# Kernel tuning notes

Measured on AMD Instinct MI355X. Metric: run time of the kernel, lower is better.

Reference implementation:

```python
import jax, jax.numpy as jnp
import numpy as np

D = 2048      # d_model
H = 32        # n_heads
DS = 64       # d_state = d_model // n_heads
K = 4         # conv kernel size (hardcoded in module)
EPS = 1e-6


def setup_inputs() -> dict:
    key = jax.random.key(0)
    ks = jax.random.split(key, 8)
    B, L = 2, 4096
    s = lambda k, shp, sc: jax.random.normal(k, shp, dtype=jnp.float32) * sc
    return {
        "x": s(ks[0], (B, L, D), 1.0),
        "state": jnp.zeros((B, H, DS), jnp.float32),
        "norm_w": jnp.ones((D,), jnp.float32),
        "conv_w": s(ks[1], (D, K), 0.5),          # depthwise conv weight [d_model, K]
        "conv_b": s(ks[2], (D,), 0.1),
        "pp_w": s(ks[3], (D, 3 * H * DS), 0.02),  # param_proj (stored [in, out])
        "pp_b": jnp.zeros((3 * H * DS,), jnp.float32),
        "gp_w": s(ks[4], (D, D), 0.02),           # gate_proj
        "gp_b": jnp.zeros((D,), jnp.float32),
        "op_w": s(ks[5], (D, D), 0.02),           # out_proj
        "op_b": jnp.zeros((D,), jnp.float32),
    }


def reference(x, state, norm_w, conv_w, conv_b, pp_w, pp_b, gp_w, gp_b, op_w, op_b):
    B, L, Dm = x.shape
    # RMSNorm
    rms = jnp.sqrt(jnp.mean(x * x, axis=-1, keepdims=True) + EPS)
    xn = norm_w * x / rms
    # causal depthwise conv1d + SiLU (pad left K-1, valid cross-correlation)
    xp = jnp.pad(xn, ((0, 0), (K - 1, 0), (0, 0)))
    xc = conv_b + sum(xp[:, k:k + L, :] * conv_w[:, k] for k in range(K))
    xc = jax.nn.silu(xc)
    gate = jax.nn.sigmoid(xc @ gp_w + gp_b)                  # [B, L, D]
    p = (xn @ pp_w + pp_b).reshape(B, L, H, 3, DS)
    delta = jax.nn.sigmoid(p[..., 0, :])                     # [B, L, H, DS]
    Bm, Cm = p[..., 1, :], p[..., 2, :]
    # sequential recurrence h_t = delta_t * h_{t-1} + B_t, time-major scan
    dt = jnp.moveaxis(delta, 1, 0)                           # [L, B, H, DS]
    Bt = jnp.moveaxis(Bm, 1, 0)
    def step(h, db):
        d, b = db
        h = d * h + b
        return h, h
    h_last, hs = jax.lax.scan(step, state, (dt, Bt))         # hs: [L, B, H, DS]
    ssm = (jnp.moveaxis(Cm, 1, 0) * hs).reshape(L, B, Dm)
    ssm = jnp.moveaxis(ssm, 0, 1)                            # [B, L, D]
    mixed = gate * ssm + (1.0 - gate) * xn
    y = mixed @ op_w + op_b + x
    return y, h_last
```

## Files before the change

### kernel.cpp

```cpp
#include <hip/hip_runtime.h>
#include <math.h>

#define BB   2
#define LL   4096
#define DD   2048
#define HH   32
#define DSS  64
#define MM   (BB * LL)
#define N3   (3 * HH * DSS)
#define NCH  64
#define CLN  64
#define EPSF 1e-6f

typedef unsigned short bf16;
typedef __attribute__((ext_vector_type(8))) short bf16x8;
typedef __attribute__((ext_vector_type(4))) float f32x4;

__device__ __forceinline__ float bf2f(bf16 u) {
    union { unsigned int i; float f; } v;
    v.i = ((unsigned int)u) << 16;
    return v.f;
}
__device__ __forceinline__ bf16 f2bf(float f) {
    union { float f; unsigned int u; } v;
    v.f = f;
    unsigned int r = (v.u >> 16) & 1u;
    return (bf16)((v.u + 0x7fffu + r) >> 16);
}
__device__ __forceinline__ float sigmoidf_(float v) {
    return 1.0f / (1.0f + __expf(-v));
}
__device__ __forceinline__ void gload16(const void* g, void* l) {
    __builtin_amdgcn_global_load_lds(
        (const __attribute__((address_space(1))) void*)g,
        (__attribute__((address_space(3))) void*)l, 16, 0, 0);
}

__global__ __launch_bounds__(256) void rms_kernel(const float* __restrict__ x,
                                                  const float* __restrict__ w,
                                                  bf16* __restrict__ xn) {
    int row = blockIdx.x;
    const float4* x4 = (const float4*)(x + (size_t)row * DD);
    ushort4* o4 = (ushort4*)(xn + (size_t)row * DD);
    const float4* w4 = (const float4*)w;
    int t = threadIdx.x;
    float4 v0 = x4[t], v1 = x4[t + 256];
    float ss = v0.x * v0.x + v0.y * v0.y + v0.z * v0.z + v0.w * v0.w +
               v1.x * v1.x + v1.y * v1.y + v1.z * v1.z + v1.w * v1.w;
#pragma unroll
    for (int off = 32; off >= 1; off >>= 1) ss += __shfl_down(ss, off, 64);
    __shared__ float red[4];
    if ((t & 63) == 0) red[t >> 6] = ss;
    __syncthreads();
    float tot = red[0] + red[1] + red[2] + red[3];
    float inv = 1.0f / sqrtf(tot * (1.0f / DD) + EPSF);
    float4 wa = w4[t], wb = w4[t + 256];
    ushort4 r0, r1;
    r0.x = f2bf(v0.x * inv * wa.x); r0.y = f2bf(v0.y * inv * wa.y);
    r0.z = f2bf(v0.z * inv * wa.z); r0.w = f2bf(v0.w * inv * wa.w);
    r1.x = f2bf(v1.x * inv * wb.x); r1.y = f2bf(v1.y * inv * wb.y);
    r1.z = f2bf(v1.z * inv * wb.z); r1.w = f2bf(v1.w * inv * wb.w);
    o4[t] = r0; o4[t + 256] = r1;
}

__global__ __launch_bounds__(256) void conv_silu_kernel(const bf16* __restrict__ xn,
                                                        const float* __restrict__ cw,
                                                        const float* __restrict__ cb,
                                                        bf16* __restrict__ xc) {
    int l = blockIdx.x;
    int b = blockIdx.y;
    size_t base = ((size_t)b * LL + l) * DD;
#pragma unroll
    for (int i = 0; i < 8; ++i) {
        int d = (i << 8) + threadIdx.x;
        float4 w = ((const float4*)cw)[d];
        float acc = cb[d];
        if (l >= 3) {
            acc += bf2f(xn[base - 3 * (size_t)DD + d]) * w.x +
                   bf2f(xn[base - 2 * (size_t)DD + d]) * w.y +
                   bf2f(xn[base - 1 * (size_t)DD + d]) * w.z +
                   bf2f(xn[base + d]) * w.w;
        } else {
            const float wv[4] = {w.x, w.y, w.z, w.w};
#pragma unroll
            for (int k = 0; k < 4; ++k) {
                int ls = l - 3 + k;
                if (ls >= 0) acc += bf2f(xn[((size_t)b * LL + ls) * DD + d]) * wv[k];
            }
        }
        xc[base + d] = f2bf(acc * sigmoidf_(acc));
    }
}

__global__ __launch_bounds__(256) void transpose_bf(const float* __restrict__ W,
                                                    bf16* __restrict__ WT,
                                                    int Kdim, int Ndim) {
    __shared__ float t[32][33];
    int n0 = blockIdx.x << 5, k0 = blockIdx.y << 5;
    int tx = threadIdx.x & 31;
    int ty = threadIdx.x >> 5;
#pragma unroll
    for (int i = 0; i < 32; i += 8)
        t[ty + i][tx] = W[(size_t)(k0 + ty + i) * Ndim + n0 + tx];
    __syncthreads();
#pragma unroll
    for (int i = 0; i < 32; i += 8)
        WT[(size_t)(n0 + ty + i) * Kdim + k0 + tx] = f2bf(t[tx][ty + i]);
}

template <int EPI, typename OutT>
__global__ __launch_bounds__(256) void gemm_mfma(const bf16* __restrict__ A,
                                                 const bf16* __restrict__ Bt,
                                                 const float* __restrict__ bias,
                                                 const float* __restrict__ add,
                                                 OutT* __restrict__ out,
                                                 int Ndim, int Kdim) {
    __shared__ __align__(16) bf16 As[128 * 64];
    __shared__ __align__(16) bf16 Bs[128 * 64];
    const int tid  = threadIdx.x;
    const int wave = tid >> 6;
    const int lane = tid & 63;
    const int m0 = blockIdx.y << 7;
    const int n0 = blockIdx.x << 7;

    const int sr = lane >> 3;
    const int gcol = ((lane & 7) ^ sr) << 3;
    const bf16* gA[4];
    const bf16* gB[4];
    bf16* lA[4];
    bf16* lB[4];
#pragma unroll
    for (int p = 0; p < 4; ++p) {
        int c = wave * 4 + p;
        gA[p] = A  + (size_t)(m0 + c * 8 + sr) * Kdim + gcol;
        gB[p] = Bt + (size_t)(n0 + c * 8 + sr) * Kdim + gcol;
        lA[p] = As + c * 512 + lane * 8;
        lB[p] = Bs + c * 512 + lane * 8;
    }

    const int wm = (wave >> 1) << 6;
    const int wn = (wave & 1) << 6;
    const int fr = lane & 15;
    const int kg = lane >> 4;
    const int f7 = fr & 7;

    f32x4 acc[4][4] = {};
    for (int k0 = 0; k0 < Kdim; k0 += 64) {
        __syncthreads();
#pragma unroll
        for (int p = 0; p < 4; ++p) {
            gload16(gA[p] + k0, lA[p]);
            gload16(gB[p] + k0, lB[p]);
        }
        __syncthreads();
#pragma unroll
        for (int ks = 0; ks < 2; ++ks) {
            bf16x8 af[4], bf_[4];
#pragma unroll
            for (int i = 0; i < 4; ++i) {
                int gq = (((ks << 2) | kg) ^ f7) << 3;
                af[i]  = *(const bf16x8*)&As[(wm + i * 16 + fr) * 64 + gq];
                bf_[i] = *(const bf16x8*)&Bs[(wn + i * 16 + fr) * 64 + gq];
            }
#pragma unroll
            for (int i = 0; i < 4; ++i)
#pragma unroll
                for (int j = 0; j < 4; ++j)
                    acc[i][j] = __builtin_amdgcn_mfma_f32_16x16x32_bf16(
                        af[i], bf_[j], acc[i][j], 0, 0, 0);
        }
    }

    const int baseRow = m0 + wm + kg * 4;
    const int baseCol = n0 + wn + fr;
#pragma unroll
    for (int i = 0; i < 4; ++i) {
#pragma unroll
        for (int r = 0; r < 4; ++r) {
            int m = baseRow + i * 16 + r;
            size_t rowoff = (size_t)m * Ndim + baseCol;
#pragma unroll
            for (int j = 0; j < 4; ++j) {
                float v = acc[i][j][r] + bias[baseCol + j * 16];
                if (EPI == 1) v = sigmoidf_(v);
                if (EPI == 2) v += add[rowoff + j * 16];
                if constexpr (sizeof(OutT) == 4)
                    ((float*)out)[rowoff + j * 16] = v;
                else
                    ((bf16*)out)[rowoff + j * 16] = f2bf(v);
            }
        }
    }
}


__global__ __launch_bounds__(256) void scan_phase1(const bf16* __restrict__ p,
                                                   float* __restrict__ cA,
                                                   float* __restrict__ cB) {
    int c = blockIdx.x, b = blockIdx.z, s = threadIdx.x & 63;
    int h = blockIdx.y * 4 + (threadIdx.x >> 6);
    size_t base = ((size_t)(b * LL + c * CLN)) * N3 + h * (3 * DSS) + s;
    float a = 1.0f, bb = 0.0f;
    for (int i = 0; i < CLN; ++i) {
        float d = sigmoidf_(bf2f(p[base]));
        float Bv = bf2f(p[base + DSS]);
        a *= d;
        bb = d * bb + Bv;
        base += N3;
    }
    int idx = ((b * HH + h) * NCH + c) * DSS + s;
    cA[idx] = a;
    cB[idx] = bb;
}

__global__ __launch_bounds__(64) void scan_phase2(const float* __restrict__ state,
                                                  const float* __restrict__ cA,
                                                  const float* __restrict__ cB,
                                                  float* __restrict__ cH,
                                                  float* __restrict__ hlast) {
    int h = blockIdx.x, b = blockIdx.y, s = threadIdx.x;
    float hp = state[(b * HH + h) * DSS + s];
    int base = ((b * HH + h) * NCH) * DSS + s;
    for (int c = 0; c < NCH; ++c) {
        cH[base + c * DSS] = hp;
        hp = cA[base + c * DSS] * hp + cB[base + c * DSS];
    }
    hlast[(b * HH + h) * DSS + s] = hp;
}

__global__ __launch_bounds__(256) void scan_phase3(const bf16* __restrict__ p,
                                                   const float* __restrict__ cH,
                                                   const bf16* __restrict__ gate,
                                                   const bf16* __restrict__ xn,
                                                   bf16* __restrict__ mixed) {
    int c = blockIdx.x, b = blockIdx.z, s = threadIdx.x & 63;
    int h = blockIdx.y * 4 + (threadIdx.x >> 6);
    float hp = cH[((b * HH + h) * NCH + c) * DSS + s];
    size_t prow = ((size_t)(b * LL + c * CLN)) * N3 + h * (3 * DSS) + s;
    size_t grow = ((size_t)(b * LL + c * CLN)) * DD + h * DSS + s;
    for (int i = 0; i < CLN; ++i) {
        float d = sigmoidf_(bf2f(p[prow]));
        float Bv = bf2f(p[prow + DSS]);
        float Cv = bf2f(p[prow + 2 * DSS]);
        hp = d * hp + Bv;
        float ssm = Cv * hp;
        float g = bf2f(gate[grow]);
        float xv = bf2f(xn[grow]);
        mixed[grow] = f2bf(g * ssm + (1.0f - g) * xv);
        prow += N3;
        grow += DD;
    }
}

extern "C" void kernel_launch(void* const* d_in, const int* in_sizes, int n_in,
                              void* d_out, int out_size, void* d_ws, size_t ws_size,
                              hipStream_t stream) {
    const float* x      = (const float*)d_in[0];
    const float* state  = (const float*)d_in[1];
    const float* norm_w = (const float*)d_in[2];
    const float* conv_w = (const float*)d_in[3];
    const float* conv_b = (const float*)d_in[4];
    const float* pp_w   = (const float*)d_in[5];
    const float* pp_b   = (const float*)d_in[6];
    const float* gp_w   = (const float*)d_in[7];
    const float* gp_b   = (const float*)d_in[8];
    const float* op_w   = (const float*)d_in[9];
    const float* op_b   = (const float*)d_in[10];

    float* y     = (float*)d_out;
    float* hlast = y + (size_t)MM * DD;

    const size_t BHND = (size_t)BB * HH * NCH * DSS;
    char* ws = (char*)d_ws;
    bf16* xn    = (bf16*)ws;
    bf16* xcbuf = xn + (size_t)MM * DD;
    bf16* p     = xcbuf + (size_t)MM * DD;
    float* cA   = (float*)(p + (size_t)MM * N3);
    float* cB   = cA + BHND;
    float* cH   = cB + BHND;
    bf16* gp_wT = (bf16*)(cH + BHND);
    bf16* op_wT = gp_wT + (size_t)DD * DD;
    bf16* pp_wT = xcbuf;
    bf16* gate  = (bf16*)y;
    bf16* mixed = xcbuf;

    rms_kernel<<<MM, 256, 0, stream>>>(x, norm_w, xn);
    conv_silu_kernel<<<dim3(LL, BB), 256, 0, stream>>>(xn, conv_w, conv_b, xcbuf);
    transpose_bf<<<dim3(DD / 32, DD / 32), 256, 0, stream>>>(gp_w, gp_wT, DD, DD);
    gemm_mfma<1, bf16><<<dim3(DD / 128, MM / 128), 256, 0, stream>>>(
        xcbuf, gp_wT, gp_b, nullptr, gate, DD, DD);
    transpose_bf<<<dim3(N3 / 32, DD / 32), 256, 0, stream>>>(pp_w, pp_wT, DD, N3);
    gemm_mfma<0, bf16><<<dim3(N3 / 128, MM / 128), 256, 0, stream>>>(
        xn, pp_wT, pp_b, nullptr, p, N3, DD);
    scan_phase1<<<dim3(NCH, HH / 4, BB), 256, 0, stream>>>(p, cA, cB);
    scan_phase2<<<dim3(HH, BB), 64, 0, stream>>>(state, cA, cB, cH, hlast);
    scan_phase3<<<dim3(NCH, HH / 4, BB), 256, 0, stream>>>(p, cH, gate, xn, mixed);
    transpose_bf<<<dim3(DD / 32, DD / 32), 256, 0, stream>>>(op_w, op_wT, DD, DD);
    gemm_mfma<2, float><<<dim3(DD / 128, MM / 128), 256, 0, stream>>>(
        mixed, op_wT, op_b, x, y, DD, DD);
}
```

Baseline: 701.2 us.

## Fuse gate and param projection GEMMs, merge weight transposes, stream conv along L

The gate-projection and param-projection GEMMs now run as a single launch, with blocks dispatched by column index, and the three weight transposes are combined into one kernel. The depthwise conv now walks 32 timesteps per thread with a register sliding window and 4-wide vector loads, so each input row is not reloaded four times. The pp_wT scratch buffer moves into the unused half of the output buffer so that it no longer aliases xc. The aims are fewer launches, better GPU fill, and less redundant memory traffic in the conv; the costs are more complex buffer aliasing and lower parallelism in the conv grid.

```diff
diff --git a/kernel.cpp b/kernel.cpp
--- a/kernel.cpp
+++ b/kernel.cpp
@@ -11,6 +11,8 @@
 #define NCH  64
 #define CLN  64
 #define EPSF 1e-6f
+#define GP_NB (DD / 128)
+#define PP_NB (N3 / 128)
 
 typedef unsigned short bf16;
 typedef __attribute__((ext_vector_type(8))) short bf16x8;
@@ -63,40 +65,67 @@
     o4[t] = r0; o4[t + 256] = r1;
 }
 
+#define CONV_LC 32
 __global__ __launch_bounds__(256) void conv_silu_kernel(const bf16* __restrict__ xn,
                                                         const float* __restrict__ cw,
                                                         const float* __restrict__ cb,
                                                         bf16* __restrict__ xc) {
-    int l = blockIdx.x;
-    int b = blockIdx.y;
-    size_t base = ((size_t)b * LL + l) * DD;
-#pragma unroll
-    for (int i = 0; i < 8; ++i) {
-        int d = (i << 8) + threadIdx.x;
-        float4 w = ((const float4*)cw)[d];
-        float acc = cb[d];
-        if (l >= 3) {
-            acc += bf2f(xn[base - 3 * (size_t)DD + d]) * w.x +
-                   bf2f(xn[base - 2 * (size_t)DD + d]) * w.y +
-                   bf2f(xn[base - 1 * (size_t)DD + d]) * w.z +
-                   bf2f(xn[base + d]) * w.w;
+    int b = blockIdx.z;
+    int l0 = blockIdx.x * CONV_LC;
+    int d0 = blockIdx.y * 1024 + threadIdx.x * 4;
+    float4 w[4];
+    float bias[4];
+#pragma unroll
+    for (int j = 0; j < 4; ++j) {
+        w[j] = ((const float4*)cw)[d0 + j];
+        bias[j] = cb[d0 + j];
+    }
+    float win[3][4];
+#pragma unroll
+    for (int k = 0; k < 3; ++k) {
+        int l = l0 - 3 + k;
+        if (l >= 0) {
+            ushort4 v = *(const ushort4*)&xn[((size_t)b * LL + l) * DD + d0];
+            win[k][0] = bf2f(v.x); win[k][1] = bf2f(v.y);
+            win[k][2] = bf2f(v.z); win[k][3] = bf2f(v.w);
         } else {
-            const float wv[4] = {w.x, w.y, w.z, w.w};
-#pragma unroll
-            for (int k = 0; k < 4; ++k) {
-                int ls = l - 3 + k;
-                if (ls >= 0) acc += bf2f(xn[((size_t)b * LL + ls) * DD + d]) * wv[k];
-            }
-        }
-        xc[base + d] = f2bf(acc * sigmoidf_(acc));
-    }
-}
-
-__global__ __launch_bounds__(256) void transpose_bf(const float* __restrict__ W,
-                                                    bf16* __restrict__ WT,
-                                                    int Kdim, int Ndim) {
+            win[k][0] = win[k][1] = win[k][2] = win[k][3] = 0.0f;
+        }
+    }
+    size_t off = ((size_t)b * LL + l0) * DD + d0;
+    for (int i = 0; i < CONV_LC; ++i) {
+        ushort4 v = *(const ushort4*)&xn[off];
+        float cur[4] = {bf2f(v.x), bf2f(v.y), bf2f(v.z), bf2f(v.w)};
+        ushort4 o;
+#pragma unroll
+        for (int j = 0; j < 4; ++j) {
+            float acc = bias[j] + win[0][j] * w[j].x + win[1][j] * w[j].y +
+                        win[2][j] * w[j].z + cur[j] * w[j].w;
+            float s = acc * sigmoidf_(acc);
+            ((unsigned short*)&o)[j] = f2bf(s);
+        }
+        *(ushort4*)&xc[off] = o;
+#pragma unroll
+        for (int j = 0; j < 4; ++j) {
+            win[0][j] = win[1][j]; win[1][j] = win[2][j]; win[2][j] = cur[j];
+        }
+        off += DD;
+    }
+}
+
+__global__ __launch_bounds__(256) void transpose3(const float* __restrict__ gp_w,
+                                                  const float* __restrict__ op_w,
+                                                  const float* __restrict__ pp_w,
+                                                  bf16* __restrict__ gp_wT,
+                                                  bf16* __restrict__ op_wT,
+                                                  bf16* __restrict__ pp_wT) {
     __shared__ float t[32][33];
-    int n0 = blockIdx.x << 5, k0 = blockIdx.y << 5;
+    int bx = blockIdx.x;
+    const float* W; bf16* WT; int Ndim;
+    if (bx < 64)       { W = gp_w; WT = gp_wT; Ndim = DD; }
+    else if (bx < 128) { W = op_w; WT = op_wT; Ndim = DD; bx -= 64; }
+    else               { W = pp_w; WT = pp_wT; Ndim = N3; bx -= 128; }
+    int n0 = bx << 5, k0 = blockIdx.y << 5;
     int tx = threadIdx.x & 31;
     int ty = threadIdx.x >> 5;
 #pragma unroll
@@ -105,24 +134,20 @@
     __syncthreads();
 #pragma unroll
     for (int i = 0; i < 32; i += 8)
-        WT[(size_t)(n0 + ty + i) * Kdim + k0 + tx] = f2bf(t[tx][ty + i]);
+        WT[(size_t)(n0 + ty + i) * DD + k0 + tx] = f2bf(t[tx][ty + i]);
 }
 
 template <int EPI, typename OutT>
-__global__ __launch_bounds__(256) void gemm_mfma(const bf16* __restrict__ A,
-                                                 const bf16* __restrict__ Bt,
-                                                 const float* __restrict__ bias,
-                                                 const float* __restrict__ add,
-                                                 OutT* __restrict__ out,
-                                                 int Ndim, int Kdim) {
-    __shared__ __align__(16) bf16 As[128 * 64];
-    __shared__ __align__(16) bf16 Bs[128 * 64];
+__device__ __forceinline__ void gemm_tile(const bf16* __restrict__ A,
+                                          const bf16* __restrict__ Bt,
+                                          const float* __restrict__ bias,
+                                          const float* __restrict__ add,
+                                          OutT* __restrict__ out,
+                                          int Ndim, int m0, int n0,
+                                          bf16* As, bf16* Bs) {
     const int tid  = threadIdx.x;
     const int wave = tid >> 6;
     const int lane = tid & 63;
-    const int m0 = blockIdx.y << 7;
-    const int n0 = blockIdx.x << 7;
-
     const int sr = lane >> 3;
     const int gcol = ((lane & 7) ^ sr) << 3;
     const bf16* gA[4];
@@ -132,12 +157,11 @@
 #pragma unroll
     for (int p = 0; p < 4; ++p) {
         int c = wave * 4 + p;
-        gA[p] = A  + (size_t)(m0 + c * 8 + sr) * Kdim + gcol;
-        gB[p] = Bt + (size_t)(n0 + c * 8 + sr) * Kdim + gcol;
+        gA[p] = A  + (size_t)(m0 + c * 8 + sr) * DD + gcol;
+        gB[p] = Bt + (size_t)(n0 + c * 8 + sr) * DD + gcol;
         lA[p] = As + c * 512 + lane * 8;
         lB[p] = Bs + c * 512 + lane * 8;
     }
-
     const int wm = (wave >> 1) << 6;
     const int wn = (wave & 1) << 6;
     const int fr = lane & 15;
@@ -145,7 +169,7 @@
     const int f7 = fr & 7;
 
     f32x4 acc[4][4] = {};
-    for (int k0 = 0; k0 < Kdim; k0 += 64) {
+    for (int k0 = 0; k0 < DD; k0 += 64) {
         __syncthreads();
 #pragma unroll
         for (int p = 0; p < 4; ++p) {
@@ -170,7 +194,6 @@
                         af[i], bf_[j], acc[i][j], 0, 0, 0);
         }
     }
-
     const int baseRow = m0 + wm + kg * 4;
     const int baseCol = n0 + wn + fr;
 #pragma unroll
@@ -193,6 +216,36 @@
     }
 }
 
+__global__ __launch_bounds__(256) void gemm_gateproj(const bf16* __restrict__ xc,
+                                                     const bf16* __restrict__ gp_wT,
+                                                     const float* __restrict__ gp_b,
+                                                     bf16* __restrict__ gate,
+                                                     const bf16* __restrict__ xn,
+                                                     const bf16* __restrict__ pp_wT,
+                                                     const float* __restrict__ pp_b,
+                                                     bf16* __restrict__ p) {
+    __shared__ __align__(16) bf16 As[128 * 64];
+    __shared__ __align__(16) bf16 Bs[128 * 64];
+    const int m0 = blockIdx.y << 7;
+    if (blockIdx.x < GP_NB) {
+        gemm_tile<1, bf16>(xc, gp_wT, gp_b, nullptr, gate, DD,
+                           m0, blockIdx.x << 7, As, Bs);
+    } else {
+        gemm_tile<0, bf16>(xn, pp_wT, pp_b, nullptr, p, N3,
+                           m0, (blockIdx.x - GP_NB) << 7, As, Bs);
+    }
+}
+
+__global__ __launch_bounds__(256) void gemm_out(const bf16* __restrict__ mixed,
+                                                const bf16* __restrict__ op_wT,
+                                                const float* __restrict__ op_b,
+                                                const float* __restrict__ x,
+                                                float* __restrict__ y) {
+    __shared__ __align__(16) bf16 As[128 * 64];
+    __shared__ __align__(16) bf16 Bs[128 * 64];
+    gemm_tile<2, float>(mixed, op_wT, op_b, x, y, DD,
+                        blockIdx.y << 7, blockIdx.x << 7, As, Bs);
+}
 
 __global__ __launch_bounds__(256) void scan_phase1(const bf16* __restrict__ p,
                                                    float* __restrict__ cA,
@@ -280,22 +333,19 @@
     float* cH   = cB + BHND;
     bf16* gp_wT = (bf16*)(cH + BHND);
     bf16* op_wT = gp_wT + (size_t)DD * DD;
-    bf16* pp_wT = xcbuf;
     bf16* gate  = (bf16*)y;
+    bf16* pp_wT = gate + (size_t)MM * DD;
     bf16* mixed = xcbuf;
 
     rms_kernel<<<MM, 256, 0, stream>>>(x, norm_w, xn);
-    conv_silu_kernel<<<dim3(LL, BB), 256, 0, stream>>>(xn, conv_w, conv_b, xcbuf);
-    transpose_bf<<<dim3(DD / 32, DD / 32), 256, 0, stream>>>(gp_w, gp_wT, DD, DD);
-    gemm_mfma<1, bf16><<<dim3(DD / 128, MM / 128), 256, 0, stream>>>(
-        xcbuf, gp_wT, gp_b, nullptr, gate, DD, DD);
-    transpose_bf<<<dim3(N3 / 32, DD / 32), 256, 0, stream>>>(pp_w, pp_wT, DD, N3);
-    gemm_mfma<0, bf16><<<dim3(N3 / 128, MM / 128), 256, 0, stream>>>(
-        xn, pp_wT, pp_b, nullptr, p, N3, DD);
+    conv_silu_kernel<<<dim3(LL / CONV_LC, DD / 1024, BB), 256, 0, stream>>>(
+        xn, conv_w, conv_b, xcbuf);
+    transpose3<<<dim3(320, DD / 32), 256, 0, stream>>>(gp_w, op_w, pp_w,
+                                                       gp_wT, op_wT, pp_wT);
+    gemm_gateproj<<<dim3(GP_NB + PP_NB, MM / 128), 256, 0, stream>>>(
+        xcbuf, gp_wT, gp_b, gate, xn, pp_wT, pp_b, p);
     scan_phase1<<<dim3(NCH, HH / 4, BB), 256, 0, stream>>>(p, cA, cB);
     scan_phase2<<<dim3(HH, BB), 64, 0, stream>>>(state, cA, cB, cH, hlast);
     scan_phase3<<<dim3(NCH, HH / 4, BB), 256, 0, stream>>>(p, cH, gate, xn, mixed);
-    transpose_bf<<<dim3(DD / 32, DD / 32), 256, 0, stream>>>(op_w, op_wT, DD, DD);
-    gemm_mfma<2, float><<<dim3(DD / 128, MM / 128), 256, 0, stream>>>(
-        mixed, op_wT, op_b, x, y, DD, DD);
-}
+    gemm_out<<<dim3(GP_NB, MM / 128), 256, 0, stream>>>(mixed, op_wT, op_b, x, y);
+}
```

After: 682.5 us. -2.7%, faster.
